# Kernel tuning notes

Measured on AMD Instinct MI355X. Metric: run time of the kernel, lower is better.

## Reference

```python
import jax, jax.numpy as jnp
import numpy as np

N_HEAD = 16
QK_NOPE = 128
QK_ROPE = 64
QK_HEAD = QK_NOPE + QK_ROPE  # 192
V_HEAD = 128
SCALE = 1.0 / np.sqrt(QK_HEAD)


def setup_inputs() -> dict:
    key = jax.random.key(0)
    ks = jax.random.split(key, 8)
    B, T, C = 2, 2048, 2048
    s = lambda fan: 1.0 / np.sqrt(fan)
    return {
        "x": jax.random.normal(ks[0], (B, T, C), jnp.float32),
        "freqs_cis": jax.random.uniform(ks[1], (T, QK_ROPE // 2, 2), jnp.float32),
        "w_q": jax.random.normal(ks[2], (C, N_HEAD * QK_HEAD), jnp.float32) * s(C),
        "w_kv_down": jax.random.normal(ks[3], (C, 256), jnp.float32) * s(C),
        "w_k_up": jax.random.normal(ks[4], (256, N_HEAD * QK_HEAD), jnp.float32) * s(256),
        "w_v_up": jax.random.normal(ks[5], (256, N_HEAD * V_HEAD), jnp.float32) * s(256),
        "w_o": jax.random.normal(ks[6], (N_HEAD * V_HEAD, C), jnp.float32) * s(N_HEAD * V_HEAD),
        "start_pos": 0,
    }


def _rotate_half(x):
    x1, x2 = x[..., : x.shape[-1] // 2], x[..., x.shape[-1] // 2 :]
    return jnp.concatenate([-x2, x1], axis=-1)


def reference(x, freqs_cis, w_q, w_kv_down, w_k_up, w_v_up, w_o, start_pos):
    B, T, C = x.shape
    # low-rank MLA projections
    q = (x @ w_q).reshape(B, T, N_HEAD, QK_HEAD)
    kv = x @ w_kv_down                                  # (B,T,r)
    k = (kv @ w_k_up).reshape(B, T, N_HEAD, QK_HEAD)
    v = (kv @ w_v_up).reshape(B, T, N_HEAD, V_HEAD)

    # inline RoPE on decoupled rope dims
    q_nope, q_rope = q[..., :QK_NOPE], q[..., QK_NOPE:]
    k_nope, k_rope = k[..., :QK_NOPE], k[..., QK_NOPE:]
    freqs = freqs_cis[start_pos : start_pos + T]         # (T, 32, 2)
    cos = freqs[..., 0][None, :, None, :]                # (1,T,1,32)
    sin = freqs[..., 1][None, :, None, :]
    rep = QK_ROPE // cos.shape[-1]
    cos = jnp.tile(cos, (1, 1, 1, rep))                  # (1,T,1,64)
    sin = jnp.tile(sin, (1, 1, 1, rep))
    q_rope = q_rope * cos + _rotate_half(q_rope) * sin
    k_rope = k_rope * cos + _rotate_half(k_rope) * sin
    q = jnp.concatenate([q_nope, q_rope], axis=-1)
    k = jnp.concatenate([k_nope, k_rope], axis=-1)

    # causal SDPA with mismatched QK vs V head dims
    scores = jnp.einsum("bqhd,bkhd->bhqk", q, k) * SCALE
    causal = jnp.tril(jnp.ones((T, T), dtype=bool))
    scores = jnp.where(causal[None, None], scores, -jnp.inf)
    probs = jax.nn.softmax(scores, axis=-1)
    out = jnp.einsum("bhqk,bkhd->bqhd", probs, v)        # (B,T,H,V_HEAD)
    out = out.reshape(B, T, N_HEAD * V_HEAD)
    return out @ w_o
```

## Files before the change

### kernel.cpp

```cpp
#include <hip/hip_runtime.h>
#include <stdint.h>

typedef unsigned short u16;
typedef float f32x4 __attribute__((ext_vector_type(4)));
typedef __bf16 bf16x8 __attribute__((ext_vector_type(8)));

static __device__ __forceinline__ u16 f2bf(float f) {
  union { float f; unsigned u; } v; v.f = f;
  unsigned r = v.u + 0x7fffu + ((v.u >> 16) & 1u);
  return (u16)(r >> 16);
}
static __device__ __forceinline__ float bf2f(u16 h) {
  union { unsigned u; float f; } v; v.u = ((unsigned)h) << 16;
  return v.f;
}

#define GLD_LDS16(gp, lp) __builtin_amdgcn_global_load_lds( \
    (__attribute__((address_space(1))) void*)(gp),          \
    (__attribute__((address_space(3))) void*)(lp), 16, 0, 0)

#define MFMA16(a, b, c) __builtin_amdgcn_mfma_f32_16x16x32_bf16((a), (b), (c), 0, 0, 0)

__global__ void prep_kernel(const float* __restrict__ x, u16* __restrict__ xb,
                            const float* __restrict__ w_q, u16* __restrict__ wqT,
                            const float* __restrict__ w_kvd, u16* __restrict__ wkdT,
                            const float* __restrict__ w_ku, u16* __restrict__ wkuT,
                            const float* __restrict__ w_vu, u16* __restrict__ wvuT,
                            const float* __restrict__ w_o, u16* __restrict__ woT) {
  __shared__ float tile[32][33];
  const int bid = blockIdx.x;
  const int tx = threadIdx.x, ty = threadIdx.y;
  if (bid < 2048) {
    const int tid = ty * 32 + tx;
    const long n = 4096ll * 2048;
    const long stride = 2048ll * 256 * 4;
    for (long i = ((long)bid * 256 + tid) * 4; i < n; i += stride) {
      float4 v = *(const float4*)(x + i);
      union { u16 s[4]; uint2 u; } pk;
      pk.s[0] = f2bf(v.x); pk.s[1] = f2bf(v.y); pk.s[2] = f2bf(v.z); pk.s[3] = f2bf(v.w);
      *(uint2*)(xb + i) = pk.u;
    }
    return;
  }
  const float* W; u16* WT; int K, N, bx, by;
  int r = bid - 2048;
  if (r < 6144)        { W = w_q;   WT = wqT;  K = 2048; N = 3072; bx = r % 96; by = r / 96; }
  else if ((r -= 6144) < 512) { W = w_kvd; WT = wkdT; K = 2048; N = 256;  bx = r % 8;  by = r / 8; }
  else if ((r -= 512) < 768)  { W = w_ku;  WT = wkuT; K = 256;  N = 3072; bx = r % 96; by = r / 96; }
  else if ((r -= 768) < 512)  { W = w_vu;  WT = wvuT; K = 256;  N = 2048; bx = r % 64; by = r / 64; }
  else                 { r -= 512; W = w_o; WT = woT; K = 2048; N = 2048; bx = r % 64; by = r / 64; }
  const int n0 = bx * 32, k0 = by * 32;
#pragma unroll
  for (int i = 0; i < 32; i += 8) tile[ty + i][tx] = W[(long)(k0 + ty + i) * N + n0 + tx];
  __syncthreads();
#pragma unroll
  for (int i = 0; i < 32; i += 8)
    WT[(long)(n0 + ty + i) * K + k0 + tx] = f2bf(tile[tx][ty + i]);
}

__device__ __forceinline__ void epilogue_rope_store(
    u16* __restrict__ C, const int N, const f32x4 (*acc)[4],
    const int m0, const int wr, const int wc, const int cbase_wave,
    const int lrow, const int lg, const bool ropewin,
    const float* __restrict__ freqs, const int sp) {
#pragma unroll
  for (int mi = 0; mi < 4; mi++) {
    const int r0 = m0 + (wr << 6) + (mi << 4) + (lg << 2);
#pragma unroll
    for (int r = 0; r < 4; r++) {
      float v0 = acc[mi][0][r], v1 = acc[mi][1][r];
      float v2 = acc[mi][2][r], v3 = acc[mi][3][r];
      if (ropewin) {
        const int t = (r0 + r) & 2047;
        const float2 cs0 = *(const float2*)&freqs[((long)(sp + t) * 32 + lrow) * 2];
        const float2 cs1 = *(const float2*)&freqs[((long)(sp + t) * 32 + 16 + lrow) * 2];
        const float n0v = v0 * cs0.x - v2 * cs0.y;
        const float n1v = v1 * cs1.x - v3 * cs1.y;
        const float n2v = v2 * cs0.x + v0 * cs0.y;
        const float n3v = v3 * cs1.x + v1 * cs1.y;
        v0 = n0v; v1 = n1v; v2 = n2v; v3 = n3v;
      }
      const long ro = (long)(r0 + r) * N + cbase_wave + lrow;
      C[ro] = f2bf(v0);
      C[ro + 16] = f2bf(v1);
      C[ro + 32] = f2bf(v2);
      C[ro + 48] = f2bf(v3);
    }
  }
}

__global__ __launch_bounds__(256, 2)
void gemm_q_kvd_kernel(const u16* __restrict__ A, const u16* __restrict__ wqT,
                       const u16* __restrict__ wkdT, u16* __restrict__ qb,
                       u16* __restrict__ kvb,
                       const float* __restrict__ freqs, const int* __restrict__ sp_ptr) {
  constexpr int K = 2048;
  const int bid = blockIdx.x;
  const int xcd = bid & 7;
  const int idx = bid >> 3;
  const int m0 = ((xcd << 2) + (idx & 3)) << 7;
  const int n0raw = (idx >> 2) << 7;
  const bool is_kv = n0raw >= 3072;
  const u16* BT = is_kv ? (wkdT + (long)(n0raw - 3072) * K) : (wqT + (long)n0raw * K);
  u16* C = is_kv ? kvb : qb;
  const int N = is_kv ? 256 : 3072;
  const int c_base = is_kv ? (n0raw - 3072) : n0raw;
  __shared__ alignas(16) u16 lA[128 * 64];
  __shared__ alignas(16) u16 lB[128 * 64];
  const int tid = threadIdx.x;
  const int w = tid >> 6, l = tid & 63;
  const int wr = w >> 1, wc = w & 1;
  const int lrow = l & 15, lg = l >> 4;
  const int srow = l >> 3, scol = (l & 7) << 3;
  f32x4 acc[4][4] = {};
  for (int kt = 0; kt < K; kt += 64) {
    __syncthreads();
#pragma unroll
    for (int i = 0; i < 4; i++) {
      const int chunk = (w << 2) + i;
      const int row = (chunk << 3) + srow;
      GLD_LDS16(A + (long)(m0 + row) * K + kt + scol, &lA[chunk << 9]);
      GLD_LDS16(BT + (long)row * K + kt + scol, &lB[chunk << 9]);
    }
    __syncthreads();
#pragma unroll
    for (int kk = 0; kk < 2; kk++) {
      bf16x8 af[4], bb[4];
#pragma unroll
      for (int i = 0; i < 4; i++) {
        af[i] = *(const bf16x8*)&lA[((wr << 6) + (i << 4) + lrow) * 64 + (kk << 5) + (lg << 3)];
        bb[i] = *(const bf16x8*)&lB[((wc << 6) + (i << 4) + lrow) * 64 + (kk << 5) + (lg << 3)];
      }
#pragma unroll
      for (int mi = 0; mi < 4; mi++)
#pragma unroll
        for (int ni = 0; ni < 4; ni++)
          acc[mi][ni] = MFMA16(af[mi], bb[ni], acc[mi][ni]);
    }
  }
  const int cbase_wave = c_base + (wc << 6);
  const bool ropewin = (!is_kv) && (cbase_wave % 192 == 128);
  const int sp = sp_ptr[0];
  epilogue_rope_store(C, N, acc, m0, wr, wc, cbase_wave, lrow, lg, ropewin, freqs, sp);
}

__global__ __launch_bounds__(256, 2)
void gemm_kup_vt_kernel(const u16* __restrict__ kvb, const u16* __restrict__ wkuT,
                        const u16* __restrict__ wvuT, u16* __restrict__ kb,
                        u16* __restrict__ vTb,
                        const float* __restrict__ freqs, const int* __restrict__ sp_ptr) {
  constexpr int K = 256;
  const int bid = blockIdx.x;
  const u16 *A, *BT;
  u16* C;
  int N, m0, n0;
  bool is_k;
  if (bid < 768) {
    const int xcd = bid & 7, idx = bid >> 3;
    A = kvb; BT = wkuT; C = kb; N = 3072;
    m0 = ((xcd << 2) + (idx & 3)) << 7;
    n0 = (idx >> 2) << 7;
    is_k = true;
  } else {
    const int r = bid - 768;
    const int xcd = r & 7, idx = r >> 3;
    const int mt = (xcd << 1) + (idx & 1);
    const int rest = idx >> 1;
    const int nt = rest & 15, bz = rest >> 4;
    A = wvuT; BT = kvb + (long)bz * 2048 * 256; C = vTb + (long)bz * 2048 * 2048;
    N = 2048;
    m0 = mt << 7; n0 = nt << 7;
    is_k = false;
  }
  __shared__ alignas(16) u16 lA[128 * 64];
  __shared__ alignas(16) u16 lB[128 * 64];
  const int tid = threadIdx.x;
  const int w = tid >> 6, l = tid & 63;
  const int wr = w >> 1, wc = w & 1;
  const int lrow = l & 15, lg = l >> 4;
  const int srow = l >> 3, scol = (l & 7) << 3;
  f32x4 acc[4][4] = {};
  for (int kt = 0; kt < K; kt += 64) {
    __syncthreads();
#pragma unroll
    for (int i = 0; i < 4; i++) {
      const int chunk = (w << 2) + i;
      const int row = (chunk << 3) + srow;
      GLD_LDS16(A + (long)(m0 + row) * K + kt + scol, &lA[chunk << 9]);
      GLD_LDS16(BT + (long)(n0 + row) * K + kt + scol, &lB[chunk << 9]);
    }
    __syncthreads();
#pragma unroll
    for (int kk = 0; kk < 2; kk++) {
      bf16x8 af[4], bb[4];
#pragma unroll
      for (int i = 0; i < 4; i++) {
        af[i] = *(const bf16x8*)&lA[((wr << 6) + (i << 4) + lrow) * 64 + (kk << 5) + (lg << 3)];
        bb[i] = *(const bf16x8*)&lB[((wc << 6) + (i << 4) + lrow) * 64 + (kk << 5) + (lg << 3)];
      }
#pragma unroll
      for (int mi = 0; mi < 4; mi++)
#pragma unroll
        for (int ni = 0; ni < 4; ni++)
          acc[mi][ni] = MFMA16(af[mi], bb[ni], acc[mi][ni]);
    }
  }
  const int cbase_wave = n0 + (wc << 6);
  const bool ropewin = is_k && (cbase_wave % 192 == 128);
  const int sp = sp_ptr[0];
  epilogue_rope_store(C, N, acc, m0, wr, wc, cbase_wave, lrow, lg, ropewin, freqs, sp);
}

__global__ __launch_bounds__(256, 2)
void gemm_out_kernel(const u16* __restrict__ A, const u16* __restrict__ BT,
                     float* __restrict__ C) {
  constexpr int K = 2048, N = 2048;
  const int bid = blockIdx.x;
  const int xcd = bid & 7, idx = bid >> 3;
  const int m0 = ((xcd << 2) + (idx & 3)) << 7;
  const int n0 = (idx >> 2) << 7;
  __shared__ alignas(16) u16 lA[128 * 64];
  __shared__ alignas(16) u16 lB[128 * 64];
  const int tid = threadIdx.x;
  const int w = tid >> 6, l = tid & 63;
  const int wr = w >> 1, wc = w & 1;
  const int lrow = l & 15, lg = l >> 4;
  const int srow = l >> 3, scol = (l & 7) << 3;
  f32x4 acc[4][4] = {};
  for (int kt = 0; kt < K; kt += 64) {
    __syncthreads();
#pragma unroll
    for (int i = 0; i < 4; i++) {
      const int chunk = (w << 2) + i;
      const int row = (chunk << 3) + srow;
      GLD_LDS16(A + (long)(m0 + row) * K + kt + scol, &lA[chunk << 9]);
      GLD_LDS16(BT + (long)(n0 + row) * K + kt + scol, &lB[chunk << 9]);
    }
    __syncthreads();
#pragma unroll
    for (int kk = 0; kk < 2; kk++) {
      bf16x8 af[4], bb[4];
#pragma unroll
      for (int i = 0; i < 4; i++) {
        af[i] = *(const bf16x8*)&lA[((wr << 6) + (i << 4) + lrow) * 64 + (kk << 5) + (lg << 3)];
        bb[i] = *(const bf16x8*)&lB[((wc << 6) + (i << 4) + lrow) * 64 + (kk << 5) + (lg << 3)];
      }
#pragma unroll
      for (int mi = 0; mi < 4; mi++)
#pragma unroll
        for (int ni = 0; ni < 4; ni++)
          acc[mi][ni] = MFMA16(af[mi], bb[ni], acc[mi][ni]);
    }
  }
#pragma unroll
  for (int mi = 0; mi < 4; mi++) {
    const int r0 = m0 + (wr << 6) + (mi << 4) + (lg << 2);
#pragma unroll
    for (int ni = 0; ni < 4; ni++) {
      const int c0 = n0 + (wc << 6) + (ni << 4) + lrow;
#pragma unroll
      for (int r = 0; r < 4; r++)
        C[(long)(r0 + r) * N + c0] = acc[mi][ni][r];
    }
  }
}


__device__ __forceinline__ void attn_tile_step(
    const bf16x8* __restrict__ qf, f32x4* __restrict__ o, float* __restrict__ l_part,
    const int qrb, const int t0,
    const u16* __restrict__ Kl, const u16* __restrict__ Vl,
    u16* __restrict__ pw, const int lrow, const int lg) {
  constexpr float SCALE = 0.07216878364870323f;
  f32x4 s[4];
  __builtin_amdgcn_s_setprio(1);
#pragma unroll
  for (int tb = 0; tb < 4; tb++) {
    f32x4 a = {};
#pragma unroll
    for (int kb = 0; kb < 6; kb++) {
      bf16x8 kf = *(const bf16x8*)&Kl[((tb << 4) + lrow) * 200 + (kb << 5) + (lg << 3)];
      a = MFMA16(qf[kb], kf, a);
    }
    s[tb] = a;
  }
  __builtin_amdgcn_s_setprio(0);
#pragma unroll
  for (int tb = 0; tb < 4; tb++) {
    const int tt = t0 + (tb << 4) + lrow;
#pragma unroll
    for (int r = 0; r < 4; r++) {
      const int qrow = qrb + (lg << 2) + r;
      float p = __expf(s[tb][r] * SCALE);
      p = (tt <= qrow) ? p : 0.f;
      s[tb][r] = p;
      l_part[r] += p;
    }
  }
#pragma unroll
  for (int tb = 0; tb < 4; tb++)
#pragma unroll
    for (int r = 0; r < 4; r++)
      pw[((lg << 2) + r) * 68 + (tb << 4) + lrow] = f2bf(s[tb][r]);
  bf16x8 pf0 = *(const bf16x8*)&pw[lrow * 68 + (lg << 3)];
  bf16x8 pf1 = *(const bf16x8*)&pw[lrow * 68 + 32 + (lg << 3)];
  __builtin_amdgcn_s_setprio(1);
#pragma unroll
  for (int db = 0; db < 8; db++) {
    bf16x8 v0 = *(const bf16x8*)&Vl[((db << 4) + lrow) * 72 + (lg << 3)];
    bf16x8 v1 = *(const bf16x8*)&Vl[((db << 4) + lrow) * 72 + 32 + (lg << 3)];
    o[db] = MFMA16(pf0, v0, o[db]);
    o[db] = MFMA16(pf1, v1, o[db]);
  }
  __builtin_amdgcn_s_setprio(0);
}

__device__ __forceinline__ void attn_tile_step2(
    const bf16x8* __restrict__ qfA, const bf16x8* __restrict__ qfB,
    f32x4* __restrict__ oA, f32x4* __restrict__ oB,
    float* __restrict__ lpA, float* __restrict__ lpB,
    const int qrbA, const int qrbB, const int t0,
    const u16* __restrict__ Kl, const u16* __restrict__ Vl,
    u16* __restrict__ pwA, u16* __restrict__ pwB, const int lrow, const int lg) {
  constexpr float SCALE = 0.07216878364870323f;
  f32x4 sA[4], sB[4];
  __builtin_amdgcn_s_setprio(1);
#pragma unroll
  for (int tb = 0; tb < 4; tb++) {
    f32x4 a = {}, bq = {};
#pragma unroll
    for (int kb = 0; kb < 6; kb++) {
      bf16x8 kf = *(const bf16x8*)&Kl[((tb << 4) + lrow) * 200 + (kb << 5) + (lg << 3)];
      a = MFMA16(qfA[kb], kf, a);
      bq = MFMA16(qfB[kb], kf, bq);
    }
    sA[tb] = a;
    sB[tb] = bq;
  }
  __builtin_amdgcn_s_setprio(0);
#pragma unroll
  for (int tb = 0; tb < 4; tb++) {
    const int tt = t0 + (tb << 4) + lrow;
#pragma unroll
    for (int r = 0; r < 4; r++) {
      const int qrowA = qrbA + (lg << 2) + r;
      float pA = __expf(sA[tb][r] * SCALE);
      pA = (tt <= qrowA) ? pA : 0.f;
      sA[tb][r] = pA;
      lpA[r] += pA;
      const int qrowB = qrbB + (lg << 2) + r;
      float pB = __expf(sB[tb][r] * SCALE);
      pB = (tt <= qrowB) ? pB : 0.f;
      sB[tb][r] = pB;
      lpB[r] += pB;
    }
  }
#pragma unroll
  for (int tb = 0; tb < 4; tb++)
#pragma unroll
    for (int r = 0; r < 4; r++) {
      pwA[((lg << 2) + r) * 68 + (tb << 4) + lrow] = f2bf(sA[tb][r]);
      pwB[((lg << 2) + r) * 68 + (tb << 4) + lrow] = f2bf(sB[tb][r]);
    }
  bf16x8 pfA0 = *(const bf16x8*)&pwA[lrow * 68 + (lg << 3)];
  bf16x8 pfA1 = *(const bf16x8*)&pwA[lrow * 68 + 32 + (lg << 3)];
  bf16x8 pfB0 = *(const bf16x8*)&pwB[lrow * 68 + (lg << 3)];
  bf16x8 pfB1 = *(const bf16x8*)&pwB[lrow * 68 + 32 + (lg << 3)];
  __builtin_amdgcn_s_setprio(1);
#pragma unroll
  for (int db = 0; db < 8; db++) {
    bf16x8 v0 = *(const bf16x8*)&Vl[((db << 4) + lrow) * 72 + (lg << 3)];
    bf16x8 v1 = *(const bf16x8*)&Vl[((db << 4) + lrow) * 72 + 32 + (lg << 3)];
    oA[db] = MFMA16(pfA0, v0, oA[db]);
    oB[db] = MFMA16(pfB0, v0, oB[db]);
    oA[db] = MFMA16(pfA1, v1, oA[db]);
    oB[db] = MFMA16(pfB1, v1, oB[db]);
  }
  __builtin_amdgcn_s_setprio(0);
}

__device__ __forceinline__ void attn_write_part(
    u16* __restrict__ op, float* __restrict__ lp,
    const f32x4* __restrict__ o, const float* __restrict__ l_part,
    const int lrow, const int lg) {
#pragma unroll
  for (int r = 0; r < 4; r++) {
    float l = l_part[r];
#pragma unroll
    for (int d = 1; d < 16; d <<= 1) l += __shfl_xor(l, d);
    if (lrow == 0) lp[(long)((lg << 2) + r) * 16] = l;
#pragma unroll
    for (int db = 0; db < 8; db++)
      op[(long)((lg << 2) + r) * 2048 + (db << 4) + lrow] = f2bf(o[db][r]);
  }
}

__global__ __launch_bounds__(256, 2)
void attn_kernel(const u16* __restrict__ q, const u16* __restrict__ k,
                 const u16* __restrict__ vT,
                 u16* __restrict__ o0p, u16* __restrict__ o1p,
                 float* __restrict__ l0p, float* __restrict__ l1p) {
  const int bid = blockIdx.x;
  const int xcd = bid & 7;
  const int rest = bid >> 3;
  const int pair = rest & 15;
  const int s = (rest >> 4) & 1;
  const int bh = ((rest >> 5) << 3) | xcd;
  const int b = bh >> 4, h = bh & 15;
  const int tid = threadIdx.x, w = tid >> 6, l = tid & 63;
  const int lrow = l & 15, lg = l >> 4;
  const int qtA = pair, qtB = 31 - pair;
  const int qrbA = (qtA << 6) + (w << 4);
  const int qrbB = (qtB << 6) + (w << 4);
  const int EA = qtA + 1, EB = qtB + 1;
  const int hA = (EA + 1) >> 1, hB = (EB + 1) >> 1;
  __shared__ alignas(16) u16 Kl[64 * 200];
  __shared__ alignas(16) u16 Vl[128 * 72];
  __shared__ alignas(16) u16 Pl[4][2][16 * 68];

  bf16x8 qfA[6], qfB[6];
  {
    const u16* qbA = q + ((long)b * 2048 + qrbA + lrow) * 3072 + h * 192;
    const u16* qbB = q + ((long)b * 2048 + qrbB + lrow) * 3072 + h * 192;
#pragma unroll
    for (int kb = 0; kb < 6; kb++) {
      qfA[kb] = *(const bf16x8*)&qbA[(kb << 5) + (lg << 3)];
      qfB[kb] = *(const bf16x8*)&qbB[(kb << 5) + (lg << 3)];
    }
  }
  f32x4 oA[8] = {}, oB[8] = {};
  float lA[4] = {}, lB[4] = {};

  const u16* kbh = k + (long)b * 2048 * 3072 + h * 192;
  const u16* vbh = vT + ((long)b * 2048 + h * 128) * 2048;

  auto stage = [&](int t0) {
    __syncthreads();
#pragma unroll
    for (int i = 0; i < 6; i++) {
      int c = (i << 8) + tid;
      int row = c / 24, col = (c % 24) << 3;
      *(bf16x8*)&Kl[row * 200 + col] = *(const bf16x8*)&kbh[(long)(t0 + row) * 3072 + col];
    }
#pragma unroll
    for (int i = 0; i < 4; i++) {
      int c = (i << 8) + tid;
      int row = c >> 3, col = (c & 7) << 3;
      *(bf16x8*)&Vl[row * 72 + col] = *(const bf16x8*)&vbh[(long)row * 2048 + t0 + col];
    }
    __syncthreads();
  };

  if (s == 0) {
    for (int T = 0; T < hB; T++) {
      const int t0 = T << 6;
      stage(t0);
      if (T < hA)
        attn_tile_step2(qfA, qfB, oA, oB, lA, lB, qrbA, qrbB, t0, Kl, Vl,
                        &Pl[w][0][0], &Pl[w][1][0], lrow, lg);
      else
        attn_tile_step(qfB, oB, lB, qrbB, t0, Kl, Vl, &Pl[w][1][0], lrow, lg);
    }
  } else {
    for (int T = hA; T < EA; T++) {
      const int t0 = T << 6;
      stage(t0);
      attn_tile_step(qfA, oA, lA, qrbA, t0, Kl, Vl, &Pl[w][0][0], lrow, lg);
    }
    for (int T = hB; T < EB; T++) {
      const int t0 = T << 6;
      stage(t0);
      attn_tile_step(qfB, oB, lB, qrbB, t0, Kl, Vl, &Pl[w][1][0], lrow, lg);
    }
  }
  u16* op = s ? o1p : o0p;
  float* lp = s ? l1p : l0p;
  attn_write_part(op + ((long)b * 2048 + qrbA) * 2048 + (h << 7),
                  lp + ((long)b * 2048 + qrbA) * 16 + h, oA, lA, lrow, lg);
  attn_write_part(op + ((long)b * 2048 + qrbB) * 2048 + (h << 7),
                  lp + ((long)b * 2048 + qrbB) * 16 + h, oB, lB, lrow, lg);
}

__global__ void attn_norm_kernel(const u16* __restrict__ o0, const u16* __restrict__ o1,
                                 const float* __restrict__ l0, const float* __restrict__ l1,
                                 u16* __restrict__ aob) {
  const long i8 = ((long)blockIdx.x * 256 + threadIdx.x) << 3;
  const int row = (int)(i8 >> 11);
  const int h = ((int)i8 & 2047) >> 7;
  const float linv = 1.f / (l0[row * 16 + h] + l1[row * 16 + h]);
  union { u16 s[8]; uint4 u; } pa, pb, po;
  pa.u = *(const uint4*)(o0 + i8);
  pb.u = *(const uint4*)(o1 + i8);
#pragma unroll
  for (int j = 0; j < 8; j++)
    po.s[j] = f2bf((bf2f(pa.s[j]) + bf2f(pb.s[j])) * linv);
  *(uint4*)(aob + i8) = po.u;
}

extern "C" void kernel_launch(void* const* d_in, const int* in_sizes, int n_in,
                              void* d_out, int out_size, void* d_ws, size_t ws_size,
                              hipStream_t stream) {
  const float* x = (const float*)d_in[0];
  const float* fcis = (const float*)d_in[1];
  const float* w_q = (const float*)d_in[2];
  const float* w_kvd = (const float*)d_in[3];
  const float* w_ku = (const float*)d_in[4];
  const float* w_vu = (const float*)d_in[5];
  const float* w_o = (const float*)d_in[6];
  const int* start_pos = (const int*)d_in[7];
  float* out = (float*)d_out;

  char* p = (char*)d_ws;
  auto alloc = [&](long bytes) -> char* {
    char* r = p;
    p += (bytes + 255) & ~255ll;
    return r;
  };
  u16* xb = (u16*)alloc(4096ll * 2048 * 2);
  u16* qb = (u16*)alloc(4096ll * 3072 * 2);
  u16* kb = (u16*)alloc(4096ll * 3072 * 2);
  u16* aob = (u16*)alloc(4096ll * 2048 * 2);
  u16* woT = (u16*)alloc(2048ll * 2048 * 2);
  char* pool = p;
  u16* wqT = (u16*)alloc(3072ll * 2048 * 2);
  u16* wkdT = (u16*)alloc(256ll * 2048 * 2);
  u16* wkuT = (u16*)alloc(3072ll * 256 * 2);
  u16* wvuT = (u16*)alloc(2048ll * 256 * 2);
  u16* kvb = (u16*)alloc(4096ll * 256 * 2);
  u16* o0p = (u16*)pool;
  u16* o1p = (u16*)(pool + 16777216);
  float* l0p = (float*)(pool + 2 * 16777216);
  float* l1p = (float*)(pool + 2 * 16777216 + 262144);
  {
    char* endp = pool + 2 * 16777216 + 2 * 262144;
    if (endp > p) p = endp;
  }
  u16* vTb = xb;

  prep_kernel<<<14080, dim3(32, 8), 0, stream>>>(x, xb, w_q, wqT, w_kvd, wkdT,
                                                 w_ku, wkuT, w_vu, wvuT, w_o, woT);
  gemm_q_kvd_kernel<<<832, 256, 0, stream>>>(xb, wqT, wkdT, qb, kvb, fcis, start_pos);
  gemm_kup_vt_kernel<<<1280, 256, 0, stream>>>(kvb, wkuT, wvuT, kb, vTb, fcis, start_pos);
  attn_kernel<<<1024, 256, 0, stream>>>(qb, kb, vTb, o0p, o1p, l0p, l1p);
  attn_norm_kernel<<<4096, 256, 0, stream>>>(o0p, o1p, l0p, l1p, aob);
  gemm_out_kernel<<<512, 256, 0, stream>>>(aob, woT, out);
}
```

Measured before the change: 278.3 us.

## Stage attention K/V via direct global-to-LDS loads with XOR-swizzled layout

Replaces the register round-trip K/V staging in the attention kernel with global_load_lds direct copies. Because those copies write LDS contiguously per wave, the padded row strides are replaced by an XOR swizzle on 16-byte chunks to keep reads bank-conflict free. The two per-wave P scratch buffers are merged into one, which shrinks LDS use. The aim is fewer VGPRs and instructions per stage and possibly higher occupancy, at the cost of serialising the A/B P writes through one buffer.

```diff
diff --git a/kernel.cpp b/kernel.cpp
--- a/kernel.cpp
+++ b/kernel.cpp
@@ -266,12 +266,17 @@
 }
 
 
+__device__ __forceinline__ const u16* kaddr(const u16* Kl, int tb, int lrow, int jr_sw) {
+  return &Kl[((tb << 4) + lrow) * 192 + (jr_sw << 3)];
+}
+
 __device__ __forceinline__ void attn_tile_step(
     const bf16x8* __restrict__ qf, f32x4* __restrict__ o, float* __restrict__ l_part,
     const int qrb, const int t0,
     const u16* __restrict__ Kl, const u16* __restrict__ Vl,
     u16* __restrict__ pw, const int lrow, const int lg) {
   constexpr float SCALE = 0.07216878364870323f;
+  const int ks = lrow & 7;
   f32x4 s[4];
   __builtin_amdgcn_s_setprio(1);
 #pragma unroll
@@ -279,7 +284,9 @@
     f32x4 a = {};
 #pragma unroll
     for (int kb = 0; kb < 6; kb++) {
-      bf16x8 kf = *(const bf16x8*)&Kl[((tb << 4) + lrow) * 200 + (kb << 5) + (lg << 3)];
+      const int jr = (kb << 2) + lg;
+      const int jr_sw = (jr & 24) | ((jr & 7) ^ ks);
+      bf16x8 kf = *(const bf16x8*)kaddr(Kl, tb, lrow, jr_sw);
       a = MFMA16(qf[kb], kf, a);
     }
     s[tb] = a;
@@ -304,11 +311,13 @@
       pw[((lg << 2) + r) * 68 + (tb << 4) + lrow] = f2bf(s[tb][r]);
   bf16x8 pf0 = *(const bf16x8*)&pw[lrow * 68 + (lg << 3)];
   bf16x8 pf1 = *(const bf16x8*)&pw[lrow * 68 + 32 + (lg << 3)];
+  const int vc0 = (lg ^ ks) << 3, vc1 = ((4 + lg) ^ ks) << 3;
   __builtin_amdgcn_s_setprio(1);
 #pragma unroll
   for (int db = 0; db < 8; db++) {
-    bf16x8 v0 = *(const bf16x8*)&Vl[((db << 4) + lrow) * 72 + (lg << 3)];
-    bf16x8 v1 = *(const bf16x8*)&Vl[((db << 4) + lrow) * 72 + 32 + (lg << 3)];
+    const int vrow = ((db << 4) + lrow) << 6;
+    bf16x8 v0 = *(const bf16x8*)&Vl[vrow + vc0];
+    bf16x8 v1 = *(const bf16x8*)&Vl[vrow + vc1];
     o[db] = MFMA16(pf0, v0, o[db]);
     o[db] = MFMA16(pf1, v1, o[db]);
   }
@@ -321,8 +330,9 @@
     float* __restrict__ lpA, float* __restrict__ lpB,
     const int qrbA, const int qrbB, const int t0,
     const u16* __restrict__ Kl, const u16* __restrict__ Vl,
-    u16* __restrict__ pwA, u16* __restrict__ pwB, const int lrow, const int lg) {
+    u16* __restrict__ pw, const int lrow, const int lg) {
   constexpr float SCALE = 0.07216878364870323f;
+  const int ks = lrow & 7;
   f32x4 sA[4], sB[4];
   __builtin_amdgcn_s_setprio(1);
 #pragma unroll
@@ -330,7 +340,9 @@
     f32x4 a = {}, bq = {};
 #pragma unroll
     for (int kb = 0; kb < 6; kb++) {
-      bf16x8 kf = *(const bf16x8*)&Kl[((tb << 4) + lrow) * 200 + (kb << 5) + (lg << 3)];
+      const int jr = (kb << 2) + lg;
+      const int jr_sw = (jr & 24) | ((jr & 7) ^ ks);
+      bf16x8 kf = *(const bf16x8*)kaddr(Kl, tb, lrow, jr_sw);
       a = MFMA16(qfA[kb], kf, a);
       bq = MFMA16(qfB[kb], kf, bq);
     }
@@ -358,19 +370,24 @@
 #pragma unroll
   for (int tb = 0; tb < 4; tb++)
 #pragma unroll
-    for (int r = 0; r < 4; r++) {
-      pwA[((lg << 2) + r) * 68 + (tb << 4) + lrow] = f2bf(sA[tb][r]);
-      pwB[((lg << 2) + r) * 68 + (tb << 4) + lrow] = f2bf(sB[tb][r]);
-    }
-  bf16x8 pfA0 = *(const bf16x8*)&pwA[lrow * 68 + (lg << 3)];
-  bf16x8 pfA1 = *(const bf16x8*)&pwA[lrow * 68 + 32 + (lg << 3)];
-  bf16x8 pfB0 = *(const bf16x8*)&pwB[lrow * 68 + (lg << 3)];
-  bf16x8 pfB1 = *(const bf16x8*)&pwB[lrow * 68 + 32 + (lg << 3)];
+    for (int r = 0; r < 4; r++)
+      pw[((lg << 2) + r) * 68 + (tb << 4) + lrow] = f2bf(sA[tb][r]);
+  bf16x8 pfA0 = *(const bf16x8*)&pw[lrow * 68 + (lg << 3)];
+  bf16x8 pfA1 = *(const bf16x8*)&pw[lrow * 68 + 32 + (lg << 3)];
+#pragma unroll
+  for (int tb = 0; tb < 4; tb++)
+#pragma unroll
+    for (int r = 0; r < 4; r++)
+      pw[((lg << 2) + r) * 68 + (tb << 4) + lrow] = f2bf(sB[tb][r]);
+  bf16x8 pfB0 = *(const bf16x8*)&pw[lrow * 68 + (lg << 3)];
+  bf16x8 pfB1 = *(const bf16x8*)&pw[lrow * 68 + 32 + (lg << 3)];
+  const int vc0 = (lg ^ ks) << 3, vc1 = ((4 + lg) ^ ks) << 3;
   __builtin_amdgcn_s_setprio(1);
 #pragma unroll
   for (int db = 0; db < 8; db++) {
-    bf16x8 v0 = *(const bf16x8*)&Vl[((db << 4) + lrow) * 72 + (lg << 3)];
-    bf16x8 v1 = *(const bf16x8*)&Vl[((db << 4) + lrow) * 72 + 32 + (lg << 3)];
+    const int vrow = ((db << 4) + lrow) << 6;
+    bf16x8 v0 = *(const bf16x8*)&Vl[vrow + vc0];
+    bf16x8 v1 = *(const bf16x8*)&Vl[vrow + vc1];
     oA[db] = MFMA16(pfA0, v0, oA[db]);
     oB[db] = MFMA16(pfB0, v0, oB[db]);
     oA[db] = MFMA16(pfA1, v1, oA[db]);
@@ -414,9 +431,9 @@
   const int qrbB = (qtB << 6) + (w << 4);
   const int EA = qtA + 1, EB = qtB + 1;
   const int hA = (EA + 1) >> 1, hB = (EB + 1) >> 1;
-  __shared__ alignas(16) u16 Kl[64 * 200];
-  __shared__ alignas(16) u16 Vl[128 * 72];
-  __shared__ alignas(16) u16 Pl[4][2][16 * 68];
+  __shared__ alignas(16) u16 Kl[64 * 192];
+  __shared__ alignas(16) u16 Vl[128 * 64];
+  __shared__ alignas(16) u16 Pl[4][16 * 68];
 
   bf16x8 qfA[6], qfB[6];
   {
@@ -434,20 +451,30 @@
   const u16* kbh = k + (long)b * 2048 * 3072 + h * 192;
   const u16* vbh = vT + ((long)b * 2048 + h * 128) * 2048;
 
+  int krow_[6], kcol_[6], vrow_[4], vcol_[4];
+#pragma unroll
+  for (int i = 0; i < 6; i++) {
+    const int c = (i << 8) + tid;
+    krow_[i] = c / 24;
+    const int j = c % 24;
+    kcol_[i] = ((j & 24) | ((j & 7) ^ (krow_[i] & 7))) << 3;
+  }
+#pragma unroll
+  for (int i = 0; i < 4; i++) {
+    const int c = (i << 8) + tid;
+    vrow_[i] = c >> 3;
+    vcol_[i] = ((c & 7) ^ (vrow_[i] & 7)) << 3;
+  }
+  const int wbase = (tid & ~63) << 3;
+
   auto stage = [&](int t0) {
     __syncthreads();
 #pragma unroll
-    for (int i = 0; i < 6; i++) {
-      int c = (i << 8) + tid;
-      int row = c / 24, col = (c % 24) << 3;
-      *(bf16x8*)&Kl[row * 200 + col] = *(const bf16x8*)&kbh[(long)(t0 + row) * 3072 + col];
-    }
-#pragma unroll
-    for (int i = 0; i < 4; i++) {
-      int c = (i << 8) + tid;
-      int row = c >> 3, col = (c & 7) << 3;
-      *(bf16x8*)&Vl[row * 72 + col] = *(const bf16x8*)&vbh[(long)row * 2048 + t0 + col];
-    }
+    for (int i = 0; i < 6; i++)
+      GLD_LDS16(kbh + (long)(t0 + krow_[i]) * 3072 + kcol_[i], &Kl[(i << 11) + wbase]);
+#pragma unroll
+    for (int i = 0; i < 4; i++)
+      GLD_LDS16(vbh + (long)vrow_[i] * 2048 + t0 + vcol_[i], &Vl[(i << 11) + wbase]);
     __syncthreads();
   };
 
@@ -457,20 +484,20 @@
       stage(t0);
       if (T < hA)
         attn_tile_step2(qfA, qfB, oA, oB, lA, lB, qrbA, qrbB, t0, Kl, Vl,
-                        &Pl[w][0][0], &Pl[w][1][0], lrow, lg);
+                        &Pl[w][0], lrow, lg);
       else
-        attn_tile_step(qfB, oB, lB, qrbB, t0, Kl, Vl, &Pl[w][1][0], lrow, lg);
+        attn_tile_step(qfB, oB, lB, qrbB, t0, Kl, Vl, &Pl[w][0], lrow, lg);
     }
   } else {
     for (int T = hA; T < EA; T++) {
       const int t0 = T << 6;
       stage(t0);
-      attn_tile_step(qfA, oA, lA, qrbA, t0, Kl, Vl, &Pl[w][0][0], lrow, lg);
+      attn_tile_step(qfA, oA, lA, qrbA, t0, Kl, Vl, &Pl[w][0], lrow, lg);
     }
     for (int T = hB; T < EB; T++) {
       const int t0 = T << 6;
       stage(t0);
-      attn_tile_step(qfB, oB, lB, qrbB, t0, Kl, Vl, &Pl[w][1][0], lrow, lg);
+      attn_tile_step(qfB, oB, lB, qrbB, t0, Kl, Vl, &Pl[w][0], lrow, lg);
     }
   }
   u16* op = s ? o1p : o0p;
```

After: 271.2 us. -2.6%, faster.
